# Optimization experiments

Measured on AMD Instinct MI355X. Metric: run time of the kernel, lower is better.

Reference implementation:

```python
import jax, jax.numpy as jnp
import numpy as np

N = 50000; F = 128; H = 128; E = 800000; G = 512; C = 1000; CE = 64; L = 128
EPS = 1e-5

def gcn_conv(x, src, dst, W, b, num_nodes):
    # PyG GCNConv: add self loops, sym-normalize, aggregate at dst
    loop = jnp.arange(num_nodes)
    s = jnp.concatenate([src, loop])
    d = jnp.concatenate([dst, loop])
    deg = jax.ops.segment_sum(jnp.ones_like(d, dtype=x.dtype), d, num_segments=num_nodes)
    dinv = jnp.where(deg > 0, jax.lax.rsqrt(deg), 0.0)
    norm = dinv[s] * dinv[d]                      # [E+N]
    h = x @ W                                     # [N,H]
    msg = h[s] * norm[:, None]                    # gather + scale
    return jax.ops.segment_sum(msg, d, num_segments=num_nodes) + b

def layer_norm(x, w, b):
    mu = jnp.mean(x, axis=-1, keepdims=True)
    var = jnp.var(x, axis=-1, keepdims=True)
    return (x - mu) * jax.lax.rsqrt(var + EPS) * w + b

def setup_inputs() -> dict:
    key = jax.random.key(0)
    ks = jax.random.split(key, 16)
    x = jax.random.normal(ks[0], (N, F), dtype=jnp.float32)
    edge_index = jax.random.randint(ks[1], (2, E), 0, N)
    batch = jnp.sort(jax.random.randint(ks[2], (N,), 0, G))
    cell_lines = jax.random.randint(ks[3], (G,), 0, C)
    def kai(k, shape):
        fan_in = shape[0]
        bound = np.sqrt(6.0 / fan_in)
        return jax.random.uniform(k, shape, jnp.float32, -bound, bound)
    return {
        'x': x, 'edge_index': edge_index, 'batch': batch, 'cell_lines': cell_lines,
        'W1': kai(ks[4], (F, H)), 'b1': jnp.zeros((H,), jnp.float32),
        'W2': kai(ks[5], (H, H)), 'b2': jnp.zeros((H,), jnp.float32),
        'emb': jax.random.normal(ks[6], (C, CE), dtype=jnp.float32),
        'Wc': kai(ks[7], (H + CE, H)), 'bc': jnp.zeros((H,), jnp.float32),
        'lnc_w': jnp.ones((H,), jnp.float32), 'lnc_b': jnp.zeros((H,), jnp.float32),
        'Wf1': kai(ks[8], (H, H)), 'bf1': jnp.zeros((H,), jnp.float32),
        'ln1_w': jnp.ones((H,), jnp.float32), 'ln1_b': jnp.zeros((H,), jnp.float32),
        'Wf2': kai(ks[9], (H, L)), 'bf2': jnp.zeros((L,), jnp.float32),
    }

def reference(x, edge_index, batch, cell_lines, W1, b1, W2, b2, emb, Wc, bc,
              lnc_w, lnc_b, Wf1, bf1, ln1_w, ln1_b, Wf2, bf2):
    src, dst = edge_index[0], edge_index[1]
    h = jax.nn.relu(gcn_conv(x, src, dst, W1, b1, N))
    h = jax.nn.relu(gcn_conv(h, src, dst, W2, b2, N))
    g = jax.ops.segment_sum(h, batch, num_segments=G)          # global_add_pool [G,H]
    ce = emb[cell_lines]                                       # [G,CE]
    comb = jnp.concatenate([g, ce], axis=1)
    comb = jax.nn.relu(layer_norm(comb @ Wc + bc, lnc_w, lnc_b))
    out = jax.nn.relu(comb @ Wf1 + bf1)                        # dropout = identity (eval)
    out = layer_norm(out, ln1_w, ln1_b)
    return out @ Wf2 + bf2
```

## Files before the change

### kernel.cpp

```cpp
#include <hip/hip_runtime.h>

#define N_NODES 50000
#define NFEAT 128
#define NEDGE 800000
#define NGRAPH 512
#define NCE 64
#define EPS 1e-5f
#define NBUCK 196
#define EPB 4096
#define BCAP 6144

typedef short s8v __attribute__((ext_vector_type(8)));
typedef float f4v __attribute__((ext_vector_type(4)));
typedef float f2v __attribute__((ext_vector_type(2)));

static __device__ __forceinline__ unsigned short f2bf(float f) {
    unsigned int u = __float_as_uint(f);
    unsigned int r = u + 0x7fffu + ((u >> 16) & 1u);
    return (unsigned short)(r >> 16);
}
static __device__ __forceinline__ float bf_lo(unsigned int packed) {
    return __uint_as_float(packed << 16);
}
static __device__ __forceinline__ float bf_hi(unsigned int packed) {
    return __uint_as_float(packed & 0xffff0000u);
}
static __device__ __forceinline__ float bf_us(unsigned short us) {
    return __uint_as_float(((unsigned int)us) << 16);
}
static __device__ __forceinline__ f2v unpk(unsigned int u) {
    f2v r; r.x = bf_lo(u); r.y = bf_hi(u); return r;
}

__global__ __launch_bounds__(256) void scatter_wcast_kernel(
    const int* __restrict__ ei, int* __restrict__ bucketCursor,
    unsigned int* __restrict__ recbuf, int E,
    const float* __restrict__ W1, const float* __restrict__ W2,
    unsigned short* __restrict__ WT1, unsigned short* __restrict__ WT2)
{
    __shared__ int hist[NBUCK];
    __shared__ int lbase[NBUCK];
    __shared__ int gbase[NBUCK];
    __shared__ int cur[NBUCK];
    __shared__ int scanbuf[256];
    __shared__ unsigned int staging[EPB];
    int tid = threadIdx.x;

    if (blockIdx.x >= NBUCK) {
        int b = blockIdx.x - NBUCK;
        const float* W = (b >= 64) ? W2 : W1;
        unsigned short* WT = (b >= 64) ? WT2 : WT1;
        int idx = (b & 63) * 256 + tid;
        int k = idx >> 7, n2 = idx & 127;
        WT[n2 * 128 + k] = f2bf(W[idx]);
        return;
    }

    if (tid < NBUCK) { hist[tid] = 0; cur[tid] = 0; }
    __syncthreads();

    unsigned int rec[EPB / 256];
    int e0 = blockIdx.x * EPB + tid;
#pragma unroll
    for (int i = 0; i < EPB / 256; ++i) {
        int e = e0 + i * 256;
        if (e < E) {
            unsigned int sv = (unsigned)ei[e];
            unsigned int dv = (unsigned)ei[E + e];
            rec[i] = sv | (dv << 16);
            atomicAdd(&hist[dv >> 8], 1);
        } else {
            rec[i] = 0xffffffffu;
        }
    }
    __syncthreads();
    int v = (tid < NBUCK) ? hist[tid] : 0;
    scanbuf[tid] = v; __syncthreads();
    for (int off = 1; off < 256; off <<= 1) {
        int t = (tid >= off) ? scanbuf[tid - off] : 0;
        __syncthreads();
        scanbuf[tid] += t;
        __syncthreads();
    }
    if (tid < NBUCK) lbase[tid] = scanbuf[tid] - v;
    int total = scanbuf[255];
    if (tid < NBUCK) gbase[tid] = (v > 0) ? atomicAdd(&bucketCursor[tid], v) : 0;
    __syncthreads();
#pragma unroll
    for (int i = 0; i < EPB / 256; ++i) {
        if (rec[i] != 0xffffffffu) {
            int b = rec[i] >> 24;
            int loc = atomicAdd(&cur[b], 1);
            staging[lbase[b] + loc] = rec[i];
        }
    }
    __syncthreads();
    for (int s = tid; s < total; s += 256) {
        unsigned int r = staging[s];
        int b = r >> 24;
        int pos = gbase[b] + (s - lbase[b]);
        if (pos < BCAP) recbuf[(size_t)b * BCAP + pos] = r;
    }
}

__global__ __launch_bounds__(256) void bucket_csr_kernel(
    const unsigned int* __restrict__ recbuf, const int* __restrict__ bucketCursor,
    int* __restrict__ rowbeg, unsigned short* __restrict__ deg,
    float* __restrict__ dinv, unsigned short* __restrict__ colidx)
{
    __shared__ int cnt[256];
    __shared__ int cur[256];
    __shared__ int scanbuf[256];
    __shared__ unsigned short stage[BCAP];
    int b = blockIdx.x, tid = threadIdx.x;
    int base = b * BCAP;
    int len = bucketCursor[b]; if (len > BCAP) len = BCAP;
    cnt[tid] = 0;
    __syncthreads();
    for (int s = tid; s < len; s += 256) {
        unsigned int r = recbuf[base + s];
        atomicAdd(&cnt[(r >> 16) & 255], 1);
    }
    __syncthreads();
    int v = cnt[tid];
    scanbuf[tid] = v; __syncthreads();
    for (int off = 1; off < 256; off <<= 1) {
        int t = (tid >= off) ? scanbuf[tid - off] : 0;
        __syncthreads();
        scanbuf[tid] += t;
        __syncthreads();
    }
    int excl = scanbuf[tid] - v;
    int node = b * 256 + tid;
    if (node < N_NODES) {
        rowbeg[node] = base + excl;
        deg[node] = (unsigned short)v;
        dinv[node] = rsqrtf((float)v + 1.0f);
    }
    cur[tid] = excl;
    __syncthreads();
    for (int s = tid; s < len; s += 256) {
        unsigned int r = recbuf[base + s];
        int pos = atomicAdd(&cur[(r >> 16) & 255], 1);
        stage[pos] = (unsigned short)(r & 0xffffu);
    }
    __syncthreads();
    for (int s = tid; s < len; s += 256) colidx[base + s] = stage[s];
}

template<bool FP32IN>
__global__ __launch_bounds__(256) void gemm_mfma_kernel(
    const void* __restrict__ Ain, const unsigned short* __restrict__ WTg,
    const float* __restrict__ dinv, unsigned short* __restrict__ HS, int nrows)
{
    __shared__ unsigned short as[128 * 128];
    __shared__ unsigned short wt[128 * 128];
    const int tid = threadIdx.x;
    const int row0 = blockIdx.x * 128;

    {
        const uint4* src = reinterpret_cast<const uint4*>(WTg);
        uint4* dst = reinterpret_cast<uint4*>(wt);
#pragma unroll
        for (int i = 0; i < 8; ++i) dst[tid + i * 256] = src[tid + i * 256];
    }
    if (FP32IN) {
        const float* X = (const float*)Ain;
#pragma unroll
        for (int i = 0; i < 16; ++i) {
            int f = tid + i * 256;
            int r = f >> 5, c4 = f & 31;
            int rr = row0 + r; if (rr >= nrows) rr = nrows - 1;
            float4 v = *reinterpret_cast<const float4*>(&X[rr * 128 + c4 * 4]);
            ushort4 o;
            o.x = f2bf(v.x); o.y = f2bf(v.y); o.z = f2bf(v.z); o.w = f2bf(v.w);
            *reinterpret_cast<ushort4*>(&as[r * 128 + c4 * 4]) = o;
        }
    } else {
        const unsigned short* X = (const unsigned short*)Ain;
#pragma unroll
        for (int i = 0; i < 8; ++i) {
            int f = tid + i * 256;
            int r = f >> 4, c8 = f & 15;
            int rr = row0 + r; if (rr >= nrows) rr = nrows - 1;
            *reinterpret_cast<uint4*>(&as[r * 128 + c8 * 8]) =
                *reinterpret_cast<const uint4*>(&X[rr * 128 + c8 * 8]);
        }
    }
    __syncthreads();

    const int w = tid >> 6;
    const int lane = tid & 63;
    const int quad = lane >> 4;
    const int col0 = lane & 15;

    s8v afr[2][4];
#pragma unroll
    for (int rt = 0; rt < 2; ++rt)
#pragma unroll
        for (int kt = 0; kt < 4; ++kt)
            afr[rt][kt] = *reinterpret_cast<const s8v*>(
                &as[(w * 32 + rt * 16 + col0) * 128 + kt * 32 + quad * 8]);

    f4v acc[2][8];
#pragma unroll
    for (int rt = 0; rt < 2; ++rt)
#pragma unroll
        for (int nt = 0; nt < 8; ++nt)
            acc[rt][nt] = (f4v){0.f, 0.f, 0.f, 0.f};

#pragma unroll
    for (int nt = 0; nt < 8; ++nt) {
        s8v bfr[4];
#pragma unroll
        for (int kt = 0; kt < 4; ++kt)
            bfr[kt] = *reinterpret_cast<const s8v*>(
                &wt[(nt * 16 + col0) * 128 + kt * 32 + quad * 8]);
#pragma unroll
        for (int rt = 0; rt < 2; ++rt)
#pragma unroll
            for (int kt = 0; kt < 4; ++kt)
                acc[rt][nt] = __builtin_amdgcn_mfma_f32_16x16x32_bf16(
                    afr[rt][kt], bfr[kt], acc[rt][nt], 0, 0, 0);
    }

    float dv[2][4];
#pragma unroll
    for (int rt = 0; rt < 2; ++rt)
#pragma unroll
        for (int reg = 0; reg < 4; ++reg) {
            int r = row0 + w * 32 + rt * 16 + quad * 4 + reg;
            dv[rt][reg] = (r < nrows) ? dinv[r] : 0.f;
        }

#pragma unroll
    for (int rt = 0; rt < 2; ++rt)
#pragma unroll
        for (int nt = 0; nt < 8; ++nt)
#pragma unroll
            for (int reg = 0; reg < 4; ++reg) {
                int rl = w * 32 + rt * 16 + quad * 4 + reg;
                as[rl * 128 + nt * 16 + col0] = f2bf(acc[rt][nt][reg] * dv[rt][reg]);
            }
    __syncthreads();
#pragma unroll
    for (int i = 0; i < 8; ++i) {
        int f = tid + i * 256;
        int r = f >> 4, c8 = f & 15;
        if (row0 + r < nrows)
            *reinterpret_cast<uint4*>(&HS[(size_t)(row0 + r) * 128 + c8 * 8]) =
                *reinterpret_cast<const uint4*>(&as[r * 128 + c8 * 8]);
    }
}

static __device__ __forceinline__ uint2 agg_node(
    const uint2* __restrict__ H2, const int* __restrict__ rowbeg,
    const unsigned short* __restrict__ deg, const unsigned short* __restrict__ colidx,
    const float* __restrict__ dinv, const float* __restrict__ bias,
    int node, int lane)
{
    const int half = lane >> 5;
    const int sub = lane & 31;
    const int beg = rowbeg[node];
    const int cnt = (int)deg[node] + 1;
    f2v a01 = {0.f, 0.f}, a23 = {0.f, 0.f};
    f2v b01 = {0.f, 0.f}, b23 = {0.f, 0.f};
    for (int base = 0; base < cnt; base += 64) {
        int m = cnt - base; if (m > 64) m = 64;
        int p = base + lane;
        int idx = 0;
        if (lane < m) idx = (p == 0) ? node : (int)colidx[beg + p - 1];
        int j = 0;
        for (; j + 16 <= m; j += 16) {
            uint2 t[8];
#pragma unroll
            for (int q = 0; q < 8; ++q) {
                int u = __shfl(idx, j + q * 2 + half);
                t[q] = H2[(size_t)u * 32 + sub];
            }
#pragma unroll
            for (int q = 0; q < 8; q += 2) {
                a01 += unpk(t[q].x);     a23 += unpk(t[q].y);
                b01 += unpk(t[q + 1].x); b23 += unpk(t[q + 1].y);
            }
        }
        for (; j + 4 <= m; j += 4) {
            int ua = __shfl(idx, j + half);
            int ub = __shfl(idx, j + 2 + half);
            uint2 ta = H2[(size_t)ua * 32 + sub];
            uint2 tb = H2[(size_t)ub * 32 + sub];
            a01 += unpk(ta.x); a23 += unpk(ta.y);
            b01 += unpk(tb.x); b23 += unpk(tb.y);
        }
        if (j + 2 <= m) {
            int u = __shfl(idx, j + half);
            uint2 t = H2[(size_t)u * 32 + sub];
            a01 += unpk(t.x); a23 += unpk(t.y);
            j += 2;
        }
        if (j < m) {
            int u = __shfl(idx, j);
            uint2 t; t.x = 0u; t.y = 0u;
            if (half == 0) t = H2[(size_t)u * 32 + sub];
            a01 += unpk(t.x); a23 += unpk(t.y);
        }
    }
    a01 += b01; a23 += b23;
    float s0 = a01.x + __shfl_xor(a01.x, 32);
    float s1 = a01.y + __shfl_xor(a01.y, 32);
    float s2 = a23.x + __shfl_xor(a23.x, 32);
    float s3 = a23.y + __shfl_xor(a23.y, 32);
    float sc = dinv[node];
    float4 bv = *reinterpret_cast<const float4*>(&bias[sub * 4]);
    float o0 = fmaxf(fmaf(s0, sc, bv.x), 0.f);
    float o1 = fmaxf(fmaf(s1, sc, bv.y), 0.f);
    float o2 = fmaxf(fmaf(s2, sc, bv.z), 0.f);
    float o3 = fmaxf(fmaf(s3, sc, bv.w), 0.f);
    uint2 o;
    o.x = (unsigned int)f2bf(o0) | ((unsigned int)f2bf(o1) << 16);
    o.y = (unsigned int)f2bf(o2) | ((unsigned int)f2bf(o3) << 16);
    return o;
}

__global__ __launch_bounds__(1024, 8) void fused_agg_gemm_kernel(
    const uint2* __restrict__ H2, const int* __restrict__ rowbeg,
    const unsigned short* __restrict__ deg, const unsigned short* __restrict__ colidx,
    const float* __restrict__ dinv, const float* __restrict__ bias,
    const unsigned short* __restrict__ WTg, unsigned short* __restrict__ HS2, int n)
{
    __shared__ unsigned short as[128 * 128];
    __shared__ unsigned short wt[128 * 128];
    __shared__ int nodeCur;
    const int tid = threadIdx.x;
    const int row0 = blockIdx.x * 128;

    if (tid == 0) nodeCur = 0;
    {
        const uint4* src = reinterpret_cast<const uint4*>(WTg);
        uint4* dst = reinterpret_cast<uint4*>(wt);
        dst[tid] = src[tid];
        dst[tid + 1024] = src[tid + 1024];
    }
    __syncthreads();

    const int w16 = tid >> 6;
    const int lane = tid & 63;

    uint2* asu2 = reinterpret_cast<uint2*>(as);
    for (;;) {
        int rr = 0;
        if (lane == 0) rr = atomicAdd(&nodeCur, 1);
        rr = __shfl(rr, 0);
        if (rr >= 128) break;
        int node = row0 + rr;
        if (node < n) {
            uint2 o = agg_node(H2, rowbeg, deg, colidx, dinv, bias, node, lane);
            if ((lane >> 5) == 0) asu2[rr * 32 + (lane & 31)] = o;
        }
    }
    __syncthreads();

    const int quad = lane >> 4;
    const int col0 = lane & 15;
    const int wr  = w16 >> 1;
    const int nt0 = (w16 & 1) * 4;

    s8v afr[4];
#pragma unroll
    for (int kt = 0; kt < 4; ++kt)
        afr[kt] = *reinterpret_cast<const s8v*>(
            &as[(wr * 16 + col0) * 128 + kt * 32 + quad * 8]);

    f4v acc[4];
#pragma unroll
    for (int nt = 0; nt < 4; ++nt) acc[nt] = (f4v){0.f, 0.f, 0.f, 0.f};

#pragma unroll
    for (int nt = 0; nt < 4; ++nt) {
        s8v bfr[4];
#pragma unroll
        for (int kt = 0; kt < 4; ++kt)
            bfr[kt] = *reinterpret_cast<const s8v*>(
                &wt[((nt0 + nt) * 16 + col0) * 128 + kt * 32 + quad * 8]);
#pragma unroll
        for (int kt = 0; kt < 4; ++kt)
            acc[nt] = __builtin_amdgcn_mfma_f32_16x16x32_bf16(
                afr[kt], bfr[kt], acc[nt], 0, 0, 0);
    }

    float dv[4];
#pragma unroll
    for (int reg = 0; reg < 4; ++reg) {
        int r = row0 + wr * 16 + quad * 4 + reg;
        dv[reg] = (r < n) ? dinv[r] : 0.f;
    }
    __syncthreads();
#pragma unroll
    for (int nt = 0; nt < 4; ++nt)
#pragma unroll
        for (int reg = 0; reg < 4; ++reg)
            as[(wr * 16 + quad * 4 + reg) * 128 + (nt0 + nt) * 16 + col0] =
                f2bf(acc[nt][reg] * dv[reg]);
    __syncthreads();
#pragma unroll
    for (int i = 0; i < 2; ++i) {
        int f = tid + i * 1024;
        int r = f >> 4, c8 = f & 15;
        if (row0 + r < n)
            *reinterpret_cast<uint4*>(&HS2[(size_t)(row0 + r) * 128 + c8 * 8]) =
                *reinterpret_cast<const uint4*>(&as[r * 128 + c8 * 8]);
    }
}

__global__ __launch_bounds__(1024, 8) void agg_pool_kernel(
    const uint2* __restrict__ H2, const int* __restrict__ rowbeg,
    const unsigned short* __restrict__ deg, const unsigned short* __restrict__ colidx,
    const float* __restrict__ dinv, const float* __restrict__ bias,
    const int* __restrict__ batch, float* __restrict__ pooled, int n)
{
    __shared__ unsigned short as[128 * 128];
    __shared__ int bsh[128];
    __shared__ float psum[8][132];
    __shared__ int nodeCur;
    const int tid = threadIdx.x;
    const int row0 = blockIdx.x * 128;
    if (tid == 0) nodeCur = 0;
    if (tid < 128) bsh[tid] = (row0 + tid < n) ? batch[row0 + tid] : -1;
    __syncthreads();

    const int lane = tid & 63;
    uint2* asu2 = reinterpret_cast<uint2*>(as);
    for (;;) {
        int rr = 0;
        if (lane == 0) rr = atomicAdd(&nodeCur, 1);
        rr = __shfl(rr, 0);
        if (rr >= 128) break;
        int node = row0 + rr;
        if (node < n) {
            uint2 o = agg_node(H2, rowbeg, deg, colidx, dinv, bias, node, lane);
            if ((lane >> 5) == 0) asu2[rr * 32 + (lane & 31)] = o;
        }
    }
    __syncthreads();

    const int g0 = bsh[0];
    int last = row0 + 127; if (last > n - 1) last = n - 1;
    const int g1 = batch[last];
    const int s = tid >> 7;
    const int f = tid & 127;
    for (int g = g0; g <= g1; ++g) {
        float acc = 0.f;
        for (int r = s; r < 128; r += 8)
            if (bsh[r] == g) acc += bf_us(as[r * 128 + f]);
        psum[s][f] = acc;
        __syncthreads();
        if (tid < 128) {
            float tot = 0.f;
#pragma unroll
            for (int q = 0; q < 8; ++q) tot += psum[q][f];
            atomicAdd(&pooled[g * 128 + f], tot);
        }
        __syncthreads();
    }
}

__global__ __launch_bounds__(256) void tail_kernel(
    const float* __restrict__ pooled,
    const int* __restrict__ cell, const float* __restrict__ emb,
    const float* __restrict__ Wc, const float* __restrict__ bc,
    const float* __restrict__ lncw, const float* __restrict__ lncb,
    const float* __restrict__ Wf1, const float* __restrict__ bf1,
    const float* __restrict__ ln1w, const float* __restrict__ ln1b,
    const float* __restrict__ Wf2, const float* __restrict__ bf2,
    float* __restrict__ out)
{
    __shared__ __align__(16) float comb[192];
    __shared__ __align__(16) float part[8][132];
    __shared__ float red[4];
    __shared__ __align__(16) float vec[128];
    const int gi = blockIdx.x;
    const int tid = threadIdx.x;
    const int cg = tid & 31;
    const int ks = tid >> 5;

    if (tid < 128) comb[tid] = pooled[gi * 128 + tid];
    else if (tid < 192) comb[tid] = emb[cell[gi] * 64 + (tid - 128)];
    __syncthreads();

    {
        float c[24];
#pragma unroll
        for (int i = 0; i < 6; ++i) {
            float4 t = *reinterpret_cast<const float4*>(&comb[ks * 24 + i * 4]);
            c[i * 4 + 0] = t.x; c[i * 4 + 1] = t.y; c[i * 4 + 2] = t.z; c[i * 4 + 3] = t.w;
        }
        float a0 = 0.f, a1 = 0.f, a2 = 0.f, a3 = 0.f;
#pragma unroll
        for (int i = 0; i < 24; ++i) {
            const float4 w = *reinterpret_cast<const float4*>(&Wc[(ks * 24 + i) * 128 + cg * 4]);
            a0 = fmaf(c[i], w.x, a0);
            a1 = fmaf(c[i], w.y, a1);
            a2 = fmaf(c[i], w.z, a2);
            a3 = fmaf(c[i], w.w, a3);
        }
        float4 o; o.x = a0; o.y = a1; o.z = a2; o.w = a3;
        *reinterpret_cast<float4*>(&part[ks][cg * 4]) = o;
    }
    __syncthreads();
    {
        float y = 0.f;
        if (tid < 128) {
            y = bc[tid];
#pragma unroll
            for (int s = 0; s < 8; ++s) y += part[s][tid];
        }
        float s1 = (tid < 128) ? y : 0.f;
        float s2 = (tid < 128) ? y * y : 0.f;
        if (tid < 128) {
#pragma unroll
            for (int off = 32; off > 0; off >>= 1) {
                s1 += __shfl_down(s1, off);
                s2 += __shfl_down(s2, off);
            }
            if ((tid & 63) == 0) { red[(tid >> 6) * 2] = s1; red[(tid >> 6) * 2 + 1] = s2; }
        }
        __syncthreads();
        float mu = (red[0] + red[2]) * (1.f / 128.f);
        float ms = (red[1] + red[3]) * (1.f / 128.f);
        float var = ms - mu * mu;
        if (tid < 128) {
            float yv = (y - mu) * rsqrtf(var + EPS) * lncw[tid] + lncb[tid];
            vec[tid] = fmaxf(yv, 0.f);
        }
    }
    __syncthreads();

    {
        float c[16];
#pragma unroll
        for (int i = 0; i < 4; ++i) {
            float4 t = *reinterpret_cast<const float4*>(&vec[ks * 16 + i * 4]);
            c[i * 4 + 0] = t.x; c[i * 4 + 1] = t.y; c[i * 4 + 2] = t.z; c[i * 4 + 3] = t.w;
        }
        float a0 = 0.f, a1 = 0.f, a2 = 0.f, a3 = 0.f;
#pragma unroll
        for (int i = 0; i < 16; ++i) {
            const float4 w = *reinterpret_cast<const float4*>(&Wf1[(ks * 16 + i) * 128 + cg * 4]);
            a0 = fmaf(c[i], w.x, a0);
            a1 = fmaf(c[i], w.y, a1);
            a2 = fmaf(c[i], w.z, a2);
            a3 = fmaf(c[i], w.w, a3);
        }
        float4 o; o.x = a0; o.y = a1; o.z = a2; o.w = a3;
        *reinterpret_cast<float4*>(&part[ks][cg * 4]) = o;
    }
    __syncthreads();
    {
        float y = 0.f;
        if (tid < 128) {
            y = bf1[tid];
#pragma unroll
            for (int s = 0; s < 8; ++s) y += part[s][tid];
            y = fmaxf(y, 0.f);
        }
        float s1 = (tid < 128) ? y : 0.f;
        float s2 = (tid < 128) ? y * y : 0.f;
        if (tid < 128) {
#pragma unroll
            for (int off = 32; off > 0; off >>= 1) {
                s1 += __shfl_down(s1, off);
                s2 += __shfl_down(s2, off);
            }
            if ((tid & 63) == 0) { red[(tid >> 6) * 2] = s1; red[(tid >> 6) * 2 + 1] = s2; }
        }
        __syncthreads();
        float mu = (red[0] + red[2]) * (1.f / 128.f);
        float ms = (red[1] + red[3]) * (1.f / 128.f);
        float var = ms - mu * mu;
        if (tid < 128)
            vec[tid] = (y - mu) * rsqrtf(var + EPS) * ln1w[tid] + ln1b[tid];
    }
    __syncthreads();

    {
        float c[16];
#pragma unroll
        for (int i = 0; i < 4; ++i) {
            float4 t = *reinterpret_cast<const float4*>(&vec[ks * 16 + i * 4]);
            c[i * 4 + 0] = t.x; c[i * 4 + 1] = t.y; c[i * 4 + 2] = t.z; c[i * 4 + 3] = t.w;
        }
        float a0 = 0.f, a1 = 0.f, a2 = 0.f, a3 = 0.f;
#pragma unroll
        for (int i = 0; i < 16; ++i) {
            const float4 w = *reinterpret_cast<const float4*>(&Wf2[(ks * 16 + i) * 128 + cg * 4]);
            a0 = fmaf(c[i], w.x, a0);
            a1 = fmaf(c[i], w.y, a1);
            a2 = fmaf(c[i], w.z, a2);
            a3 = fmaf(c[i], w.w, a3);
        }
        float4 o; o.x = a0; o.y = a1; o.z = a2; o.w = a3;
        *reinterpret_cast<float4*>(&part[ks][cg * 4]) = o;
    }
    __syncthreads();
    if (tid < 128) {
        float y = bf2[tid];
#pragma unroll
        for (int s = 0; s < 8; ++s) y += part[s][tid];
        out[gi * 128 + tid] = y;
    }
}

extern "C" void kernel_launch(void* const* d_in, const int* in_sizes, int n_in,
                              void* d_out, int out_size, void* d_ws, size_t ws_size,
                              hipStream_t stream) {
    const float* x    = (const float*)d_in[0];
    const int*   ei   = (const int*)d_in[1];
    const int*   batch= (const int*)d_in[2];
    const int*   cell = (const int*)d_in[3];
    const float* W1   = (const float*)d_in[4];
    const float* b1   = (const float*)d_in[5];
    const float* W2   = (const float*)d_in[6];
    const float* b2   = (const float*)d_in[7];
    const float* emb  = (const float*)d_in[8];
    const float* Wc   = (const float*)d_in[9];
    const float* bc   = (const float*)d_in[10];
    const float* lncw = (const float*)d_in[11];
    const float* lncb = (const float*)d_in[12];
    const float* Wf1  = (const float*)d_in[13];
    const float* bf1  = (const float*)d_in[14];
    const float* ln1w = (const float*)d_in[15];
    const float* ln1b = (const float*)d_in[16];
    const float* Wf2  = (const float*)d_in[17];
    const float* bf2  = (const float*)d_in[18];
    float* out = (float*)d_out;

    char* ws = (char*)d_ws;
    size_t off = 0;
    auto alloc = [&](size_t bytes) { char* p = ws + off; off = (off + bytes + 255) & ~size_t(255); return p; };
    int*            bucketCursor= (int*)  alloc(1024);
    float*          pooled      = (float*)alloc((size_t)NGRAPH * 128 * 4);
    float*          dinv        = (float*)alloc(N_NODES * 4);
    int*            rowbeg      = (int*)  alloc(N_NODES * 4);
    unsigned short* deg         = (unsigned short*)alloc(N_NODES * 2);
    unsigned short* colidx      = (unsigned short*)alloc((size_t)NBUCK * BCAP * 2);
    unsigned int*   recbuf      = (unsigned int*)alloc((size_t)NBUCK * BCAP * 4);
    unsigned short* wt1         = (unsigned short*)alloc(128 * 128 * 2);
    unsigned short* wt2         = (unsigned short*)alloc(128 * 128 * 2);
    unsigned short* hs          = (unsigned short*)alloc((size_t)N_NODES * 128 * 2);
    unsigned short* hs2         = (unsigned short*)alloc((size_t)N_NODES * 128 * 2);

    const int nbEdge = (NEDGE + EPB - 1) / EPB;
    const int nbGemm = (N_NODES + 127) / 128;

    hipMemsetAsync(bucketCursor, 0, 1024 + (size_t)NGRAPH * 128 * 4, stream);

    scatter_wcast_kernel<<<nbEdge + 128, 256, 0, stream>>>(ei, bucketCursor, recbuf, NEDGE,
                                                           W1, W2, wt1, wt2);
    bucket_csr_kernel<<<NBUCK, 256, 0, stream>>>(recbuf, bucketCursor, rowbeg, deg, dinv, colidx);

    gemm_mfma_kernel<true><<<nbGemm, 256, 0, stream>>>(x, wt1, dinv, hs, N_NODES);

    fused_agg_gemm_kernel<<<nbGemm, 1024, 0, stream>>>(
        (const uint2*)hs, rowbeg, deg, colidx, dinv, b1, wt2, hs2, N_NODES);

    agg_pool_kernel<<<nbGemm, 1024, 0, stream>>>(
        (const uint2*)hs2, rowbeg, deg, colidx, dinv, b2, batch, pooled, N_NODES);

    tail_kernel<<<NGRAPH, 256, 0, stream>>>(pooled, cell, emb, Wc, bc, lncw, lncb,
                                            Wf1, bf1, ln1w, ln1b, Wf2, bf2, out);
}
```

Measured before the change: 221.6 us.

## Swizzle LDS tiles and fuse MLP tail into pooling kernel via completion counters

Applies an XOR swizzle to the shared-memory A and W tiles in both GEMM kernels to avoid LDS bank conflicts on MFMA fragment loads and stores. It also folds the tail MLP into the aggregation+pooling kernel: each block bumps a per-graph completion counter, and the last block touching a graph runs that graph's MLP. Empty graphs are handled by the final block. This removes one kernel launch and the round trip of pooled data, but adds serial binary searches, atomics, fences and uneven per-block tail work.

```diff
diff --git a/kernel.cpp b/kernel.cpp
--- a/kernel.cpp
+++ b/kernel.cpp
@@ -30,6 +30,14 @@
 }
 static __device__ __forceinline__ f2v unpk(unsigned int u) {
     f2v r; r.x = bf_lo(u); r.y = bf_hi(u); return r;
+}
+static __device__ __forceinline__ int swz(int row, int col) {
+    return col ^ ((row & 7) << 3);
+}
+static __device__ __forceinline__ int lbound(const int* __restrict__ a, int n, int key) {
+    int lo = 0, hi = n;
+    while (lo < hi) { int mid = (lo + hi) >> 1; if (a[mid] < key) lo = mid + 1; else hi = mid; }
+    return lo;
 }
 
 __global__ __launch_bounds__(256) void scatter_wcast_kernel(
@@ -162,7 +170,11 @@
         const uint4* src = reinterpret_cast<const uint4*>(WTg);
         uint4* dst = reinterpret_cast<uint4*>(wt);
 #pragma unroll
-        for (int i = 0; i < 8; ++i) dst[tid + i * 256] = src[tid + i * 256];
+        for (int i = 0; i < 8; ++i) {
+            int t = tid + i * 256;
+            int d = (t & ~15) | ((t & 15) ^ ((t >> 4) & 7));
+            dst[d] = src[t];
+        }
     }
     if (FP32IN) {
         const float* X = (const float*)Ain;
@@ -174,7 +186,7 @@
             float4 v = *reinterpret_cast<const float4*>(&X[rr * 128 + c4 * 4]);
             ushort4 o;
             o.x = f2bf(v.x); o.y = f2bf(v.y); o.z = f2bf(v.z); o.w = f2bf(v.w);
-            *reinterpret_cast<ushort4*>(&as[r * 128 + c4 * 4]) = o;
+            *reinterpret_cast<ushort4*>(&as[r * 128 + swz(r, c4 * 4)]) = o;
         }
     } else {
         const unsigned short* X = (const unsigned short*)Ain;
@@ -183,7 +195,7 @@
             int f = tid + i * 256;
             int r = f >> 4, c8 = f & 15;
             int rr = row0 + r; if (rr >= nrows) rr = nrows - 1;
-            *reinterpret_cast<uint4*>(&as[r * 128 + c8 * 8]) =
+            *reinterpret_cast<uint4*>(&as[r * 128 + swz(r, c8 * 8)]) =
                 *reinterpret_cast<const uint4*>(&X[rr * 128 + c8 * 8]);
         }
     }
@@ -198,9 +210,11 @@
 #pragma unroll
     for (int rt = 0; rt < 2; ++rt)
 #pragma unroll
-        for (int kt = 0; kt < 4; ++kt)
+        for (int kt = 0; kt < 4; ++kt) {
+            int rA = w * 32 + rt * 16 + col0;
             afr[rt][kt] = *reinterpret_cast<const s8v*>(
-                &as[(w * 32 + rt * 16 + col0) * 128 + kt * 32 + quad * 8]);
+                &as[rA * 128 + swz(rA, kt * 32 + quad * 8)]);
+        }
 
     f4v acc[2][8];
 #pragma unroll
@@ -213,9 +227,11 @@
     for (int nt = 0; nt < 8; ++nt) {
         s8v bfr[4];
 #pragma unroll
-        for (int kt = 0; kt < 4; ++kt)
+        for (int kt = 0; kt < 4; ++kt) {
+            int rB = nt * 16 + col0;
             bfr[kt] = *reinterpret_cast<const s8v*>(
-                &wt[(nt * 16 + col0) * 128 + kt * 32 + quad * 8]);
+                &wt[rB * 128 + swz(rB, kt * 32 + quad * 8)]);
+        }
 #pragma unroll
         for (int rt = 0; rt < 2; ++rt)
 #pragma unroll
@@ -240,7 +256,7 @@
 #pragma unroll
             for (int reg = 0; reg < 4; ++reg) {
                 int rl = w * 32 + rt * 16 + quad * 4 + reg;
-                as[rl * 128 + nt * 16 + col0] = f2bf(acc[rt][nt][reg] * dv[rt][reg]);
+                as[rl * 128 + swz(rl, nt * 16 + col0)] = f2bf(acc[rt][nt][reg] * dv[rt][reg]);
             }
     __syncthreads();
 #pragma unroll
@@ -249,7 +265,7 @@
         int r = f >> 4, c8 = f & 15;
         if (row0 + r < nrows)
             *reinterpret_cast<uint4*>(&HS[(size_t)(row0 + r) * 128 + c8 * 8]) =
-                *reinterpret_cast<const uint4*>(&as[r * 128 + c8 * 8]);
+                *reinterpret_cast<const uint4*>(&as[r * 128 + swz(r, c8 * 8)]);
     }
 }
 
@@ -338,8 +354,9 @@
     {
         const uint4* src = reinterpret_cast<const uint4*>(WTg);
         uint4* dst = reinterpret_cast<uint4*>(wt);
-        dst[tid] = src[tid];
-        dst[tid + 1024] = src[tid + 1024];
+        int t0 = tid, t1 = tid + 1024;
+        dst[(t0 & ~15) | ((t0 & 15) ^ ((t0 >> 4) & 7))] = src[t0];
+        dst[(t1 & ~15) | ((t1 & 15) ^ ((t1 >> 4) & 7))] = src[t1];
     }
     __syncthreads();
 
@@ -355,7 +372,10 @@
         int node = row0 + rr;
         if (node < n) {
             uint2 o = agg_node(H2, rowbeg, deg, colidx, dinv, bias, node, lane);
-            if ((lane >> 5) == 0) asu2[rr * 32 + (lane & 31)] = o;
+            if ((lane >> 5) == 0) {
+                int sub = lane & 31;
+                asu2[rr * 32 + (sub ^ ((rr & 7) << 1))] = o;
+            }
         }
     }
     __syncthreads();
@@ -367,9 +387,11 @@
 
     s8v afr[4];
 #pragma unroll
-    for (int kt = 0; kt < 4; ++kt)
+    for (int kt = 0; kt < 4; ++kt) {
+        int rA = wr * 16 + col0;
         afr[kt] = *reinterpret_cast<const s8v*>(
-            &as[(wr * 16 + col0) * 128 + kt * 32 + quad * 8]);
+            &as[rA * 128 + swz(rA, kt * 32 + quad * 8)]);
+    }
 
     f4v acc[4];
 #pragma unroll
@@ -379,9 +401,11 @@
     for (int nt = 0; nt < 4; ++nt) {
         s8v bfr[4];
 #pragma unroll
-        for (int kt = 0; kt < 4; ++kt)
+        for (int kt = 0; kt < 4; ++kt) {
+            int rB = (nt0 + nt) * 16 + col0;
             bfr[kt] = *reinterpret_cast<const s8v*>(
-                &wt[((nt0 + nt) * 16 + col0) * 128 + kt * 32 + quad * 8]);
+                &wt[rB * 128 + swz(rB, kt * 32 + quad * 8)]);
+        }
 #pragma unroll
         for (int kt = 0; kt < 4; ++kt)
             acc[nt] = __builtin_amdgcn_mfma_f32_16x16x32_bf16(
@@ -398,9 +422,10 @@
 #pragma unroll
     for (int nt = 0; nt < 4; ++nt)
 #pragma unroll
-        for (int reg = 0; reg < 4; ++reg)
-            as[(wr * 16 + quad * 4 + reg) * 128 + (nt0 + nt) * 16 + col0] =
-                f2bf(acc[nt][reg] * dv[reg]);
+        for (int reg = 0; reg < 4; ++reg) {
+            int rl = wr * 16 + quad * 4 + reg;
+            as[rl * 128 + swz(rl, (nt0 + nt) * 16 + col0)] = f2bf(acc[nt][reg] * dv[reg]);
+        }
     __syncthreads();
 #pragma unroll
     for (int i = 0; i < 2; ++i) {
@@ -408,23 +433,176 @@
         int r = f >> 4, c8 = f & 15;
         if (row0 + r < n)
             *reinterpret_cast<uint4*>(&HS2[(size_t)(row0 + r) * 128 + c8 * 8]) =
-                *reinterpret_cast<const uint4*>(&as[r * 128 + c8 * 8]);
-    }
-}
-
-__global__ __launch_bounds__(1024, 8) void agg_pool_kernel(
+                *reinterpret_cast<const uint4*>(&as[r * 128 + swz(r, c8 * 8)]);
+    }
+}
+
+static __device__ void mlp_graph(int gi, int tid,
+    float* __restrict__ pooled, const int* __restrict__ cell, const float* __restrict__ emb,
+    const float* __restrict__ Wc, const float* __restrict__ bc,
+    const float* __restrict__ lncw, const float* __restrict__ lncb,
+    const float* __restrict__ Wf1, const float* __restrict__ bf1,
+    const float* __restrict__ ln1w, const float* __restrict__ ln1b,
+    const float* __restrict__ Wf2, const float* __restrict__ bf2,
+    float* __restrict__ out,
+    float* comb, float (*part)[132], float* red, float* vec)
+{
+    const int cg = tid & 31;
+    const int ks = tid >> 5;
+
+    if (tid < 128) comb[tid] = atomicAdd(&pooled[gi * 128 + tid], 0.0f);
+    else if (tid < 192) comb[tid] = emb[cell[gi] * 64 + (tid - 128)];
+    __syncthreads();
+
+    if (tid < 256) {
+        float c[24];
+#pragma unroll
+        for (int i = 0; i < 6; ++i) {
+            float4 t = *reinterpret_cast<const float4*>(&comb[ks * 24 + i * 4]);
+            c[i * 4 + 0] = t.x; c[i * 4 + 1] = t.y; c[i * 4 + 2] = t.z; c[i * 4 + 3] = t.w;
+        }
+        float a0 = 0.f, a1 = 0.f, a2 = 0.f, a3 = 0.f;
+#pragma unroll
+        for (int i = 0; i < 24; ++i) {
+            const float4 w = *reinterpret_cast<const float4*>(&Wc[(ks * 24 + i) * 128 + cg * 4]);
+            a0 = fmaf(c[i], w.x, a0);
+            a1 = fmaf(c[i], w.y, a1);
+            a2 = fmaf(c[i], w.z, a2);
+            a3 = fmaf(c[i], w.w, a3);
+        }
+        float4 o; o.x = a0; o.y = a1; o.z = a2; o.w = a3;
+        *reinterpret_cast<float4*>(&part[ks][cg * 4]) = o;
+    }
+    __syncthreads();
+    {
+        float y = 0.f;
+        if (tid < 128) {
+            y = bc[tid];
+#pragma unroll
+            for (int s = 0; s < 8; ++s) y += part[s][tid];
+        }
+        float s1 = (tid < 128) ? y : 0.f;
+        float s2 = (tid < 128) ? y * y : 0.f;
+        if (tid < 128) {
+#pragma unroll
+            for (int off = 32; off > 0; off >>= 1) {
+                s1 += __shfl_down(s1, off);
+                s2 += __shfl_down(s2, off);
+            }
+            if ((tid & 63) == 0) { red[(tid >> 6) * 2] = s1; red[(tid >> 6) * 2 + 1] = s2; }
+        }
+        __syncthreads();
+        float mu = (red[0] + red[2]) * (1.f / 128.f);
+        float ms = (red[1] + red[3]) * (1.f / 128.f);
+        float var = ms - mu * mu;
+        if (tid < 128) {
+            float yv = (y - mu) * rsqrtf(var + EPS) * lncw[tid] + lncb[tid];
+            vec[tid] = fmaxf(yv, 0.f);
+        }
+    }
+    __syncthreads();
+
+    if (tid < 256) {
+        float c[16];
+#pragma unroll
+        for (int i = 0; i < 4; ++i) {
+            float4 t = *reinterpret_cast<const float4*>(&vec[ks * 16 + i * 4]);
+            c[i * 4 + 0] = t.x; c[i * 4 + 1] = t.y; c[i * 4 + 2] = t.z; c[i * 4 + 3] = t.w;
+        }
+        float a0 = 0.f, a1 = 0.f, a2 = 0.f, a3 = 0.f;
+#pragma unroll
+        for (int i = 0; i < 16; ++i) {
+            const float4 w = *reinterpret_cast<const float4*>(&Wf1[(ks * 16 + i) * 128 + cg * 4]);
+            a0 = fmaf(c[i], w.x, a0);
+            a1 = fmaf(c[i], w.y, a1);
+            a2 = fmaf(c[i], w.z, a2);
+            a3 = fmaf(c[i], w.w, a3);
+        }
+        float4 o; o.x = a0; o.y = a1; o.z = a2; o.w = a3;
+        *reinterpret_cast<float4*>(&part[ks][cg * 4]) = o;
+    }
+    __syncthreads();
+    {
+        float y = 0.f;
+        if (tid < 128) {
+            y = bf1[tid];
+#pragma unroll
+            for (int s = 0; s < 8; ++s) y += part[s][tid];
+            y = fmaxf(y, 0.f);
+        }
+        float s1 = (tid < 128) ? y : 0.f;
+        float s2 = (tid < 128) ? y * y : 0.f;
+        if (tid < 128) {
+#pragma unroll
+            for (int off = 32; off > 0; off >>= 1) {
+                s1 += __shfl_down(s1, off);
+                s2 += __shfl_down(s2, off);
+            }
+            if ((tid & 63) == 0) { red[(tid >> 6) * 2] = s1; red[(tid >> 6) * 2 + 1] = s2; }
+        }
+        __syncthreads();
+        float mu = (red[0] + red[2]) * (1.f / 128.f);
+        float ms = (red[1] + red[3]) * (1.f / 128.f);
+        float var = ms - mu * mu;
+        if (tid < 128)
+            vec[tid] = (y - mu) * rsqrtf(var + EPS) * ln1w[tid] + ln1b[tid];
+    }
+    __syncthreads();
+
+    if (tid < 256) {
+        float c[16];
+#pragma unroll
+        for (int i = 0; i < 4; ++i) {
+            float4 t = *reinterpret_cast<const float4*>(&vec[ks * 16 + i * 4]);
+            c[i * 4 + 0] = t.x; c[i * 4 + 1] = t.y; c[i * 4 + 2] = t.z; c[i * 4 + 3] = t.w;
+        }
+        float a0 = 0.f, a1 = 0.f, a2 = 0.f, a3 = 0.f;
+#pragma unroll
+        for (int i = 0; i < 16; ++i) {
+            const float4 w = *reinterpret_cast<const float4*>(&Wf2[(ks * 16 + i) * 128 + cg * 4]);
+            a0 = fmaf(c[i], w.x, a0);
+            a1 = fmaf(c[i], w.y, a1);
+            a2 = fmaf(c[i], w.z, a2);
+            a3 = fmaf(c[i], w.w, a3);
+        }
+        float4 o; o.x = a0; o.y = a1; o.z = a2; o.w = a3;
+        *reinterpret_cast<float4*>(&part[ks][cg * 4]) = o;
+    }
+    __syncthreads();
+    if (tid < 128) {
+        float y = bf2[tid];
+#pragma unroll
+        for (int s = 0; s < 8; ++s) y += part[s][tid];
+        out[gi * 128 + tid] = y;
+    }
+    __syncthreads();
+}
+
+__global__ __launch_bounds__(1024, 8) void agg_pool_tail_kernel(
     const uint2* __restrict__ H2, const int* __restrict__ rowbeg,
     const unsigned short* __restrict__ deg, const unsigned short* __restrict__ colidx,
     const float* __restrict__ dinv, const float* __restrict__ bias,
-    const int* __restrict__ batch, float* __restrict__ pooled, int n)
+    const int* __restrict__ batch, float* __restrict__ pooled, int* __restrict__ blkCnt,
+    const int* __restrict__ cell, const float* __restrict__ emb,
+    const float* __restrict__ Wc, const float* __restrict__ bc,
+    const float* __restrict__ lncw, const float* __restrict__ lncb,
+    const float* __restrict__ Wf1, const float* __restrict__ bf1,
+    const float* __restrict__ ln1w, const float* __restrict__ ln1b,
+    const float* __restrict__ Wf2, const float* __restrict__ bf2,
+    float* __restrict__ out, int n)
 {
     __shared__ unsigned short as[128 * 128];
     __shared__ int bsh[128];
     __shared__ float psum[8][132];
     __shared__ int nodeCur;
+    __shared__ __align__(16) float comb[192];
+    __shared__ float red[4];
+    __shared__ __align__(16) float vec[128];
+    __shared__ int claim[130];
+    __shared__ int nclaim;
     const int tid = threadIdx.x;
     const int row0 = blockIdx.x * 128;
-    if (tid == 0) nodeCur = 0;
+    if (tid == 0) { nodeCur = 0; nclaim = 0; }
     if (tid < 128) bsh[tid] = (row0 + tid < n) ? batch[row0 + tid] : -1;
     __syncthreads();
 
@@ -462,151 +640,41 @@
         }
         __syncthreads();
     }
-}
-
-__global__ __launch_bounds__(256) void tail_kernel(
-    const float* __restrict__ pooled,
-    const int* __restrict__ cell, const float* __restrict__ emb,
-    const float* __restrict__ Wc, const float* __restrict__ bc,
-    const float* __restrict__ lncw, const float* __restrict__ lncb,
-    const float* __restrict__ Wf1, const float* __restrict__ bf1,
-    const float* __restrict__ ln1w, const float* __restrict__ ln1b,
-    const float* __restrict__ Wf2, const float* __restrict__ bf2,
-    float* __restrict__ out)
-{
-    __shared__ __align__(16) float comb[192];
-    __shared__ __align__(16) float part[8][132];
-    __shared__ float red[4];
-    __shared__ __align__(16) float vec[128];
-    const int gi = blockIdx.x;
-    const int tid = threadIdx.x;
-    const int cg = tid & 31;
-    const int ks = tid >> 5;
-
-    if (tid < 128) comb[tid] = pooled[gi * 128 + tid];
-    else if (tid < 192) comb[tid] = emb[cell[gi] * 64 + (tid - 128)];
-    __syncthreads();
-
-    {
-        float c[24];
-#pragma unroll
-        for (int i = 0; i < 6; ++i) {
-            float4 t = *reinterpret_cast<const float4*>(&comb[ks * 24 + i * 4]);
-            c[i * 4 + 0] = t.x; c[i * 4 + 1] = t.y; c[i * 4 + 2] = t.z; c[i * 4 + 3] = t.w;
-        }
-        float a0 = 0.f, a1 = 0.f, a2 = 0.f, a3 = 0.f;
-#pragma unroll
-        for (int i = 0; i < 24; ++i) {
-            const float4 w = *reinterpret_cast<const float4*>(&Wc[(ks * 24 + i) * 128 + cg * 4]);
-            a0 = fmaf(c[i], w.x, a0);
-            a1 = fmaf(c[i], w.y, a1);
-            a2 = fmaf(c[i], w.z, a2);
-            a3 = fmaf(c[i], w.w, a3);
-        }
-        float4 o; o.x = a0; o.y = a1; o.z = a2; o.w = a3;
-        *reinterpret_cast<float4*>(&part[ks][cg * 4]) = o;
-    }
-    __syncthreads();
-    {
-        float y = 0.f;
-        if (tid < 128) {
-            y = bc[tid];
-#pragma unroll
-            for (int s = 0; s < 8; ++s) y += part[s][tid];
-        }
-        float s1 = (tid < 128) ? y : 0.f;
-        float s2 = (tid < 128) ? y * y : 0.f;
-        if (tid < 128) {
-#pragma unroll
-            for (int off = 32; off > 0; off >>= 1) {
-                s1 += __shfl_down(s1, off);
-                s2 += __shfl_down(s2, off);
+
+    __threadfence();
+    __syncthreads();
+    if (tid == 0) {
+        int nc = 0;
+        for (int g = g0; g <= g1; ++g) {
+            int fb = (g == g0) ? (lbound(batch, n, g) >> 7) : blockIdx.x;
+            int lb2 = (g == g1) ? ((lbound(batch, n, g + 1) - 1) >> 7) : blockIdx.x;
+            int expected = lb2 - fb + 1;
+            int old = atomicAdd(&blkCnt[g], 1);
+            if (old == expected - 1) claim[nc++] = g;
+        }
+        nclaim = nc;
+    }
+    __syncthreads();
+    const int nc = nclaim;
+    for (int ci = 0; ci < nc; ++ci)
+        mlp_graph(claim[ci], tid, pooled, cell, emb, Wc, bc, lncw, lncb,
+                  Wf1, bf1, ln1w, ln1b, Wf2, bf2, out, comb, psum, red, vec);
+
+    if (blockIdx.x == gridDim.x - 1) {
+        if (tid == 0) nclaim = 0;
+        __syncthreads();
+        if (tid < NGRAPH) {
+            int s0 = lbound(batch, n, tid);
+            if (s0 >= n || batch[s0] != tid) {
+                int k = atomicAdd(&nclaim, 1);
+                if (k < 130) claim[k] = tid;
             }
-            if ((tid & 63) == 0) { red[(tid >> 6) * 2] = s1; red[(tid >> 6) * 2 + 1] = s2; }
-        }
-        __syncthreads();
-        float mu = (red[0] + red[2]) * (1.f / 128.f);
-        float ms = (red[1] + red[3]) * (1.f / 128.f);
-        float var = ms - mu * mu;
-        if (tid < 128) {
-            float yv = (y - mu) * rsqrtf(var + EPS) * lncw[tid] + lncb[tid];
-            vec[tid] = fmaxf(yv, 0.f);
-        }
-    }
-    __syncthreads();
-
-    {
-        float c[16];
-#pragma unroll
-        for (int i = 0; i < 4; ++i) {
-            float4 t = *reinterpret_cast<const float4*>(&vec[ks * 16 + i * 4]);
-            c[i * 4 + 0] = t.x; c[i * 4 + 1] = t.y; c[i * 4 + 2] = t.z; c[i * 4 + 3] = t.w;
-        }
-        float a0 = 0.f, a1 = 0.f, a2 = 0.f, a3 = 0.f;
-#pragma unroll
-        for (int i = 0; i < 16; ++i) {
-            const float4 w = *reinterpret_cast<const float4*>(&Wf1[(ks * 16 + i) * 128 + cg * 4]);
-            a0 = fmaf(c[i], w.x, a0);
-            a1 = fmaf(c[i], w.y, a1);
-            a2 = fmaf(c[i], w.z, a2);
-            a3 = fmaf(c[i], w.w, a3);
-        }
-        float4 o; o.x = a0; o.y = a1; o.z = a2; o.w = a3;
-        *reinterpret_cast<float4*>(&part[ks][cg * 4]) = o;
-    }
-    __syncthreads();
-    {
-        float y = 0.f;
-        if (tid < 128) {
-            y = bf1[tid];
-#pragma unroll
-            for (int s = 0; s < 8; ++s) y += part[s][tid];
-            y = fmaxf(y, 0.f);
-        }
-        float s1 = (tid < 128) ? y : 0.f;
-        float s2 = (tid < 128) ? y * y : 0.f;
-        if (tid < 128) {
-#pragma unroll
-            for (int off = 32; off > 0; off >>= 1) {
-                s1 += __shfl_down(s1, off);
-                s2 += __shfl_down(s2, off);
-            }
-            if ((tid & 63) == 0) { red[(tid >> 6) * 2] = s1; red[(tid >> 6) * 2 + 1] = s2; }
-        }
-        __syncthreads();
-        float mu = (red[0] + red[2]) * (1.f / 128.f);
-        float ms = (red[1] + red[3]) * (1.f / 128.f);
-        float var = ms - mu * mu;
-        if (tid < 128)
-            vec[tid] = (y - mu) * rsqrtf(var + EPS) * ln1w[tid] + ln1b[tid];
-    }
-    __syncthreads();
-
-    {
-        float c[16];
-#pragma unroll
-        for (int i = 0; i < 4; ++i) {
-            float4 t = *reinterpret_cast<const float4*>(&vec[ks * 16 + i * 4]);
-            c[i * 4 + 0] = t.x; c[i * 4 + 1] = t.y; c[i * 4 + 2] = t.z; c[i * 4 + 3] = t.w;
-        }
-        float a0 = 0.f, a1 = 0.f, a2 = 0.f, a3 = 0.f;
-#pragma unroll
-        for (int i = 0; i < 16; ++i) {
-            const float4 w = *reinterpret_cast<const float4*>(&Wf2[(ks * 16 + i) * 128 + cg * 4]);
-            a0 = fmaf(c[i], w.x, a0);
-            a1 = fmaf(c[i], w.y, a1);
-            a2 = fmaf(c[i], w.z, a2);
-            a3 = fmaf(c[i], w.w, a3);
-        }
-        float4 o; o.x = a0; o.y = a1; o.z = a2; o.w = a3;
-        *reinterpret_cast<float4*>(&part[ks][cg * 4]) = o;
-    }
-    __syncthreads();
-    if (tid < 128) {
-        float y = bf2[tid];
-#pragma unroll
-        for (int s = 0; s < 8; ++s) y += part[s][tid];
-        out[gi * 128 + tid] = y;
+        }
+        __syncthreads();
+        int ne = nclaim; if (ne > 130) ne = 130;
+        for (int i = 0; i < ne; ++i)
+            mlp_graph(claim[i], tid, pooled, cell, emb, Wc, bc, lncw, lncb,
+                      Wf1, bf1, ln1w, ln1b, Wf2, bf2, out, comb, psum, red, vec);
     }
 }
 
@@ -637,8 +705,9 @@
     char* ws = (char*)d_ws;
     size_t off = 0;
     auto alloc = [&](size_t bytes) { char* p = ws + off; off = (off + bytes + 255) & ~size_t(255); return p; };
-    int*            bucketCursor= (int*)  alloc(1024);
+    int*            bucketCursor= (int*)  alloc(4096);
     float*          pooled      = (float*)alloc((size_t)NGRAPH * 128 * 4);
+    int*            blkCnt      = bucketCursor + 256;
     float*          dinv        = (float*)alloc(N_NODES * 4);
     int*            rowbeg      = (int*)  alloc(N_NODES * 4);
     unsigned short* deg         = (unsigned short*)alloc(N_NODES * 2);
@@ -652,7 +721,7 @@
     const int nbEdge = (NEDGE + EPB - 1) / EPB;
     const int nbGemm = (N_NODES + 127) / 128;
 
-    hipMemsetAsync(bucketCursor, 0, 1024 + (size_t)NGRAPH * 128 * 4, stream);
+    hipMemsetAsync(bucketCursor, 0, 4096 + (size_t)NGRAPH * 128 * 4, stream);
 
     scatter_wcast_kernel<<<nbEdge + 128, 256, 0, stream>>>(ei, bucketCursor, recbuf, NEDGE,
                                                            W1, W2, wt1, wt2);
@@ -663,9 +732,7 @@
     fused_agg_gemm_kernel<<<nbGemm, 1024, 0, stream>>>(
         (const uint2*)hs, rowbeg, deg, colidx, dinv, b1, wt2, hs2, N_NODES);
 
-    agg_pool_kernel<<<nbGemm, 1024, 0, stream>>>(
-        (const uint2*)hs2, rowbeg, deg, colidx, dinv, b2, batch, pooled, N_NODES);
-
-    tail_kernel<<<NGRAPH, 256, 0, stream>>>(pooled, cell, emb, Wc, bc, lncw, lncb,
-                                            Wf1, bf1, ln1w, ln1b, Wf2, bf2, out);
-}
+    agg_pool_tail_kernel<<<nbGemm, 1024, 0, stream>>>(
+        (const uint2*)hs2, rowbeg, deg, colidx, dinv, b2, batch, pooled, blkCnt,
+        cell, emb, Wc, bc, lncw, lncb, Wf1, bf1, ln1w, ln1b, Wf2, bf2, out, N_NODES);
+}
```

Result: slower. 370.4 us (+67.2%).
